# Kernel optimization log

Hardware: AMD Instinct MI355X
Metric: run time of the kernel (lower is better)

Reference implementation:

```python
import jax, jax.numpy as jnp
import numpy as np

N, E, IN, H, OUT, G = 50000, 800000, 128, 256, 10, 512


def setup_inputs() -> dict:
    key = jax.random.key(0)
    ks = jax.random.split(key, 12)
    def lin(k, fan_in, fan_out):
        s = 1.0 / np.sqrt(fan_in)
        kw, kb = jax.random.split(k)
        W = jax.random.uniform(kw, (fan_in, fan_out), jnp.float32, -s, s)
        b = jax.random.uniform(kb, (fan_out,), jnp.float32, -s, s)
        return W, b
    x = jax.random.normal(ks[0], (N, IN), jnp.float32)
    edge_index = jax.random.randint(ks[1], (2, E), 0, N)
    batch = jnp.sort(jax.random.randint(ks[2], (N,), 0, G))
    W1a, b1a = lin(ks[3], IN, H)
    W1b, b1b = lin(ks[4], H, H)
    W2a, b2a = lin(ks[5], H, H)
    W2b, b2b = lin(ks[6], H, H)
    Wlin, blin = lin(ks[7], H, OUT)
    eps1 = jnp.zeros((), jnp.float32)
    eps2 = jnp.zeros((), jnp.float32)
    return dict(x=x, edge_index=edge_index, batch=batch,
                eps1=eps1, W1a=W1a, b1a=b1a, W1b=W1b, b1b=b1b,
                eps2=eps2, W2a=W2a, b2a=b2a, W2b=W2b, b2b=b2b,
                Wlin=Wlin, blin=blin)


def reference(x, edge_index, batch, eps1, W1a, b1a, W1b, b1b,
              eps2, W2a, b2a, W2b, b2b, Wlin, blin):
    src, dst = edge_index[0], edge_index[1]
    # GINConv 1: h = MLP((1+eps)*x + sum_{j in N(i)} x_j)
    agg = jax.ops.segment_sum(x[src], dst, num_segments=N)  # [N, IN]
    h = (1.0 + eps1) * x + agg
    h = jax.nn.relu(h @ W1a + b1a) @ W1b + b1b              # [N, H]
    h = jax.nn.relu(h)  # (dropout p=0.3 is identity in eval mode)
    # GINConv 2
    agg2 = jax.ops.segment_sum(h[src], dst, num_segments=N)  # [N, H]
    h2 = (1.0 + eps2) * h + agg2
    h2 = jax.nn.relu(h2 @ W2a + b2a) @ W2b + b2b             # [N, H]
    # global mean pool per graph
    psum = jax.ops.segment_sum(h2, batch, num_segments=G)    # [G, H]
    cnt = jax.ops.segment_sum(jnp.ones((N, 1), h2.dtype), batch, num_segments=G)
    pooled = psum / jnp.maximum(cnt, 1.0)
    out = pooled @ Wlin + blin                               # [G, OUT]
    return jax.nn.log_softmax(out, axis=-1)
```

## Files before the change

### kernel.cpp

```cpp
#include <hip/hip_runtime.h>
#include <math.h>
#include <stdint.h>

constexpr int N   = 50000;
constexpr int E   = 800000;
constexpr int IN  = 128;
constexpr int H   = 256;
constexpr int OUT = 10;
constexpr int G   = 512;
constexpr int BSTR = 64;

constexpr int NPART  = 391;
constexpr int SEGCAP = 48;
constexpr int EPB    = 4096;
constexpr int AB     = (E + EPB - 1) / EPB;

typedef __bf16 bf16x8 __attribute__((ext_vector_type(8)));
typedef float  f32x4  __attribute__((ext_vector_type(4)));
typedef float  f32x2  __attribute__((ext_vector_type(2)));

__device__ __forceinline__ float blo(unsigned v) { return __uint_as_float(v << 16); }
__device__ __forceinline__ float bhi(unsigned v) { return __uint_as_float(v & 0xffff0000u); }
__device__ __forceinline__ unsigned short f2b(float f) {
  unsigned u = __float_as_uint(f);
  u += 0x7fffu + ((u >> 16) & 1u);
  return (unsigned short)(u >> 16);
}
__device__ __forceinline__ unsigned packb(float lo, float hi) {
  return (unsigned)f2b(lo) | ((unsigned)f2b(hi) << 16);
}
__device__ __forceinline__ unsigned pk_fp8x4(float a, float b, float c, float d) {
  int r = 0;
  r = __builtin_amdgcn_cvt_pk_fp8_f32(a, b, r, false);
  r = __builtin_amdgcn_cvt_pk_fp8_f32(c, d, r, true);
  return (unsigned)r;
}
__device__ __forceinline__ unsigned char fp8_1(float v) {
  return (unsigned char)(__builtin_amdgcn_cvt_pk_fp8_f32(v, v, 0, false) & 0xff);
}

__device__ __forceinline__ void acc16(float* a, uint4 w, float s) {
  unsigned ws[4] = {w.x, w.y, w.z, w.w};
#pragma unroll
  for (int d = 0; d < 4; ++d) {
    f32x2 lo = __builtin_amdgcn_cvt_pk_f32_fp8((int)ws[d], false);
    f32x2 hi = __builtin_amdgcn_cvt_pk_f32_fp8((int)ws[d], true);
    a[4*d+0] = fmaf(s, lo.x, a[4*d+0]);
    a[4*d+1] = fmaf(s, lo.y, a[4*d+1]);
    a[4*d+2] = fmaf(s, hi.x, a[4*d+2]);
    a[4*d+3] = fmaf(s, hi.y, a[4*d+3]);
  }
}


constexpr int XQ_BLOCKS  = (N * IN / 4) / 256;
constexpr int W1A_BLOCKS = (256 * IN) / 256;
constexpr int WH_BLOCKS  = (256 * H) / 256;

__global__ __launch_bounds__(256) void prep_kernel(
    const int* __restrict__ srcp, const int* __restrict__ dstp,
    unsigned* __restrict__ pbuf, int* __restrict__ pcnt,
    const float* __restrict__ x, unsigned* __restrict__ xq,
    const float* __restrict__ W1a, unsigned short* __restrict__ Wt1a,
    const float* __restrict__ W1b, unsigned short* __restrict__ Wt1b,
    const float* __restrict__ W2a, unsigned short* __restrict__ Wt2a,
    const float* __restrict__ W2b, unsigned short* __restrict__ Wt2b) {
  __shared__ int lcur[NPART];
  int b = blockIdx.x;
  int t = threadIdx.x;
  if (b < AB) {
    for (int j = t; j < NPART; j += 256) lcur[j] = 0;
    __syncthreads();
    const int e0 = b * EPB;
#pragma unroll
    for (int r = 0; r < EPB / 1024; ++r) {
      int base = e0 + (r * 256 + t) * 4;
      if (base < E) {
        int4 d4 = *(const int4*)(dstp + base);
        int4 s4 = *(const int4*)(srcp + base);
        int dd[4] = {d4.x, d4.y, d4.z, d4.w};
        int ss[4] = {s4.x, s4.y, s4.z, s4.w};
#pragma unroll
        for (int u = 0; u < 4; ++u) {
          int part = dd[u] >> 7, dl = dd[u] & 127;
          int pos = atomicAdd(&lcur[part], 1);
          if (pos < SEGCAP)
            pbuf[((size_t)part * AB + b) * SEGCAP + pos] =
                ((unsigned)dl << 16) | (unsigned)ss[u];
        }
      }
    }
    __syncthreads();
    for (int j = t; j < NPART; j += 256) pcnt[b * NPART + j] = min(lcur[j], SEGCAP);
    return;
  }
  b -= AB;
  if (b < XQ_BLOCKS) {
    int id = b * 256 + t;
    float4 v = ((const float4*)x)[id];
    xq[id] = pk_fp8x4(v.x, v.y, v.z, v.w);
    return;
  }
  b -= XQ_BLOCKS;
  if (b < W1A_BLOCKS) {
    int id = b * 256 + t;
    int n = id >> 7, k = id & 127;
    Wt1a[id] = f2b(W1a[k * 256 + n]);
    return;
  }
  b -= W1A_BLOCKS;
  const float* Ws;
  unsigned short* Wd;
  if (b < WH_BLOCKS)            { Ws = W1b; Wd = Wt1b; }
  else if (b < 2 * WH_BLOCKS)   { Ws = W2a; Wd = Wt2a; b -= WH_BLOCKS; }
  else                          { Ws = W2b; Wd = Wt2b; b -= 2 * WH_BLOCKS; }
  int id = b * 256 + t;
  int n = id >> 8, k = id & 255;
  Wd[id] = f2b(Ws[k * 256 + n]);
}


__global__ __launch_bounds__(256) void csr_kernel(const unsigned* __restrict__ pbuf,
                                                  const int* __restrict__ pcnt,
                                                  int* __restrict__ deg, int* __restrict__ csre) {
  __shared__ int sa[256], sb[256];
  __shared__ int ldeg[128];
  int p = blockIdx.x;
  int t = threadIdx.x;
  if (t < 128) ldeg[t] = 0;
  sa[t] = (t < AB) ? pcnt[t * NPART + p] : 0;
  __syncthreads();
  int* cur = sa; int* nxt = sb;
#pragma unroll
  for (int off = 1; off < 256; off <<= 1) {
    nxt[t] = cur[t] + ((t >= off) ? cur[t - off] : 0);
    __syncthreads();
    int* tmp = cur; cur = nxt; nxt = tmp;
  }
  int T = cur[255];
  const unsigned* seg = pbuf + (size_t)p * AB * SEGCAP;
  for (int f = t; f < T; f += 256) {
    int lo = 0, hi = AB - 1;
    while (lo < hi) { int m = (lo + hi) >> 1; if (cur[m] > f) hi = m; else lo = m + 1; }
    int bb = lo;
    int excl = bb ? cur[bb - 1] : 0;
    unsigned v = seg[(size_t)bb * SEGCAP + (f - excl)];
    int dl = (int)(v >> 16), s = (int)(v & 0xFFFFu);
    int pos = atomicAdd(&ldeg[dl], 1);
    if (pos < BSTR) csre[(((size_t)p << 7) + dl) * BSTR + pos] = s;
  }
  __syncthreads();
  if (t < 128) {
    int node = (p << 7) + t;
    if (node < N) deg[node] = min(ldeg[t], BSTR);
  }
}


template <int K1, bool RELU2, bool OUT8>
__global__ __launch_bounds__(256, 3) void fused_mlp_kernel(
    const unsigned char* __restrict__ inq,
    const int* __restrict__ deg, const int* __restrict__ csre,
    const float* __restrict__ epsp,
    const unsigned short* __restrict__ Bta,
    const float* __restrict__ ba,
    const unsigned short* __restrict__ Btb,
    const float* __restrict__ bb,
    void* __restrict__ outv, int Nrows) {
  constexpr int LDK = 40;
  constexpr int LDA = K1 + 40;
  constexpr int LDI = H + 40;
  constexpr int W   = K1 / 8;
  constexpr int LPN = W / 16;
  constexpr int BATCH = 8 / LPN;
  __shared__ __align__(16) unsigned short sh[10240 + 32 * LDI];
  unsigned short* Bs = sh;
  unsigned short* Af = sh + 10240;
  unsigned short* Is = sh + 10240;
  const int tid  = threadIdx.x;
  const int r0   = blockIdx.x * 32;
  const int wave = tid >> 6, lane = tid & 63;
  const int quad = lane >> 4, l15 = lane & 15;
  const int wcol = wave * 64;
  const int srow = tid >> 2;
  const int sk8  = (tid & 3) * 8;

  {
    const float sc = 1.0f + epsp[0];
    const int slot = tid & 7;
    const int nd0  = tid >> 3;
    const unsigned char* rb = inq + slot * W;
    const int i = r0 + nd0;
    float a[W];
#pragma unroll
    for (int q = 0; q < W; ++q) a[q] = 0.f;
    if (i < Nrows) {
      int dg = deg[i]; if (dg > BSTR) dg = BSTR;
      const int* bkt = csre + (size_t)i * BSTR;
      int j = 0;
      for (; j + BATCH <= dg; j += BATCH) {
        unsigned idx[BATCH];
#pragma unroll
        for (int u = 0; u < BATCH; ++u) {
          unsigned raw = (unsigned)bkt[j + u];
          idx[u] = raw < (unsigned)N ? raw : 0u;
        }
        uint4 v[8];
#pragma unroll
        for (int u = 0; u < BATCH; ++u) {
          const uint4* src = (const uint4*)(rb + (size_t)idx[u] * K1);
#pragma unroll
          for (int p2 = 0; p2 < LPN; ++p2) v[u * LPN + p2] = src[p2];
        }
#pragma unroll
        for (int u = 0; u < BATCH; ++u)
#pragma unroll
          for (int p2 = 0; p2 < LPN; ++p2) acc16(a + 16 * p2, v[u * LPN + p2], 1.0f);
      }
      for (; j < dg; ++j) {
        unsigned raw = (unsigned)bkt[j];
        if (raw >= (unsigned)N) raw = 0u;
        const uint4* src = (const uint4*)(rb + (size_t)raw * K1);
#pragma unroll
        for (int p2 = 0; p2 < LPN; ++p2) acc16(a + 16 * p2, src[p2], 1.0f);
      }
      const uint4* sr = (const uint4*)(rb + (size_t)i * K1);
#pragma unroll
      for (int p2 = 0; p2 < LPN; ++p2) acc16(a + 16 * p2, sr[p2], sc);
    }
    uint4* dst = (uint4*)(Af + nd0 * LDA + slot * W);
#pragma unroll
    for (int w = 0; w < W / 8; ++w)
      dst[w] = make_uint4(packb(a[8*w+0], a[8*w+1]), packb(a[8*w+2], a[8*w+3]),
                          packb(a[8*w+4], a[8*w+5]), packb(a[8*w+6], a[8*w+7]));
  }

  f32x4 acc1[2][4];
#pragma unroll
  for (int i = 0; i < 2; ++i)
#pragma unroll
    for (int j = 0; j < 4; ++j) acc1[i][j] = (f32x4){0.f, 0.f, 0.f, 0.f};

  for (int k0 = 0; k0 < K1; k0 += 32) {
#pragma unroll
    for (int sgm = 0; sgm < 4; ++sgm) {
      int col = srow + sgm * 64;
      *(uint4*)(Bs + col * LDK + sk8) = *(const uint4*)(Bta + (size_t)col * K1 + k0 + sk8);
    }
    __syncthreads();
    bf16x8 af[2];
#pragma unroll
    for (int mt = 0; mt < 2; ++mt)
      af[mt] = *(const bf16x8*)(Af + (mt * 16 + l15) * LDA + k0 + quad * 8);
    bf16x8 bfr[4];
#pragma unroll
    for (int nt = 0; nt < 4; ++nt)
      bfr[nt] = *(const bf16x8*)(Bs + (wcol + nt * 16 + l15) * LDK + quad * 8);
#pragma unroll
    for (int mt = 0; mt < 2; ++mt)
#pragma unroll
      for (int nt = 0; nt < 4; ++nt)
        acc1[mt][nt] =
            __builtin_amdgcn_mfma_f32_16x16x32_bf16(af[mt], bfr[nt], acc1[mt][nt], 0, 0, 0);
    __syncthreads();
  }

  float bva[4];
#pragma unroll
  for (int nt = 0; nt < 4; ++nt) bva[nt] = ba[wcol + nt * 16 + l15];

#pragma unroll
  for (int mt = 0; mt < 2; ++mt)
#pragma unroll
    for (int nt = 0; nt < 4; ++nt) {
      int col = wcol + nt * 16 + l15;
      int rbase = mt * 16 + quad * 4;
#pragma unroll
      for (int i = 0; i < 4; ++i)
        Is[(rbase + i) * LDI + col] = f2b(fmaxf(acc1[mt][nt][i] + bva[nt], 0.f));
    }
  __syncthreads();

  f32x4 acc2[2][4];
#pragma unroll
  for (int i = 0; i < 2; ++i)
#pragma unroll
    for (int j = 0; j < 4; ++j) acc2[i][j] = (f32x4){0.f, 0.f, 0.f, 0.f};

  for (int kk = 0; kk < H / 32; ++kk) {
    const int k0 = kk * 32;
#pragma unroll
    for (int sgm = 0; sgm < 4; ++sgm) {
      int col = srow + sgm * 64;
      *(uint4*)(Bs + col * LDK + sk8) = *(const uint4*)(Btb + (size_t)col * 256 + k0 + sk8);
    }
    __syncthreads();
    bf16x8 af[2];
#pragma unroll
    for (int mt = 0; mt < 2; ++mt)
      af[mt] = *(const bf16x8*)(Is + (mt * 16 + l15) * LDI + k0 + quad * 8);
    bf16x8 bfr[4];
#pragma unroll
    for (int nt = 0; nt < 4; ++nt)
      bfr[nt] = *(const bf16x8*)(Bs + (wcol + nt * 16 + l15) * LDK + quad * 8);
#pragma unroll
    for (int mt = 0; mt < 2; ++mt)
#pragma unroll
      for (int nt = 0; nt < 4; ++nt)
        acc2[mt][nt] =
            __builtin_amdgcn_mfma_f32_16x16x32_bf16(af[mt], bfr[nt], acc2[mt][nt], 0, 0, 0);
    __syncthreads();
  }

  float bv[4];
#pragma unroll
  for (int nt = 0; nt < 4; ++nt) bv[nt] = bb[wcol + nt * 16 + l15];
#pragma unroll
  for (int mt = 0; mt < 2; ++mt) {
    int gr0 = r0 + mt * 16 + quad * 4;
#pragma unroll
    for (int i = 0; i < 4; ++i) {
      int grow = gr0 + i;
      if (grow >= Nrows) continue;
#pragma unroll
      for (int nt = 0; nt < 4; ++nt) {
        float v = acc2[mt][nt][i] + bv[nt];
        if (RELU2) v = fmaxf(v, 0.f);
        int col = wcol + nt * 16 + l15;
        if (OUT8) ((unsigned char*)outv)[(size_t)grow * 256 + col] = fp8_1(v);
        else      ((unsigned short*)outv)[(size_t)grow * 256 + col] = f2b(v);
      }
    }
  }
}


__global__ __launch_bounds__(128) void pool_final_kernel(const unsigned short* __restrict__ h2,
                                                         const int* __restrict__ batch,
                                                         const float* __restrict__ Wlin,
                                                         const float* __restrict__ blin,
                                                         float* __restrict__ out) {
  __shared__ float sp[H];
  __shared__ float logits[OUT];
  int g = blockIdx.x;
  int t = threadIdx.x;
  int lo = 0, hi = N;
  while (lo < hi) { int m = (lo + hi) >> 1; if (batch[m] < g) lo = m + 1; else hi = m; }
  int s = lo;
  lo = 0; hi = N;
  while (lo < hi) { int m = (lo + hi) >> 1; if (batch[m] < g + 1) lo = m + 1; else hi = m; }
  int e = lo;
  float a0 = 0.f, a1 = 0.f;
  const unsigned* base = (const unsigned*)h2;
  int n = s;
  for (; n + 4 <= e; n += 4) {
    unsigned v0 = base[(size_t)(n + 0) * (H / 2) + t];
    unsigned v1 = base[(size_t)(n + 1) * (H / 2) + t];
    unsigned v2 = base[(size_t)(n + 2) * (H / 2) + t];
    unsigned v3 = base[(size_t)(n + 3) * (H / 2) + t];
    a0 += blo(v0) + blo(v1) + blo(v2) + blo(v3);
    a1 += bhi(v0) + bhi(v1) + bhi(v2) + bhi(v3);
  }
  for (; n < e; ++n) {
    unsigned v = base[(size_t)n * (H / 2) + t];
    a0 += blo(v); a1 += bhi(v);
  }
  float inv = 1.0f / fmaxf((float)(e - s), 1.0f);
  sp[2 * t]     = a0 * inv;
  sp[2 * t + 1] = a1 * inv;
  __syncthreads();
  if (t < OUT) {
    float acc = blin[t];
    for (int k = 0; k < H; ++k) acc = fmaf(sp[k], Wlin[k * OUT + t], acc);
    logits[t] = acc;
  }
  __syncthreads();
  if (t == 0) {
    float m = -INFINITY;
    for (int j = 0; j < OUT; ++j) m = fmaxf(m, logits[j]);
    float ssum = 0.f;
    for (int j = 0; j < OUT; ++j) ssum += expf(logits[j] - m);
    float ls = logf(ssum);
    for (int j = 0; j < OUT; ++j) out[(size_t)g * OUT + j] = logits[j] - m - ls;
  }
}


static inline char* align_up(char* p, size_t a) {
  return (char*)(((uintptr_t)p + a - 1) & ~(a - 1));
}

extern "C" void kernel_launch(void* const* d_in, const int* in_sizes, int n_in,
                              void* d_out, int out_size, void* d_ws, size_t ws_size,
                              hipStream_t stream) {
  const float* x    = (const float*)d_in[0];
  const int*   ei   = (const int*)d_in[1];
  const int*   srcp = ei;
  const int*   dstp = ei + E;
  const int*   batch = (const int*)d_in[2];
  const float* eps1 = (const float*)d_in[3];
  const float* W1a  = (const float*)d_in[4];
  const float* b1a  = (const float*)d_in[5];
  const float* W1b  = (const float*)d_in[6];
  const float* b1b  = (const float*)d_in[7];
  const float* eps2 = (const float*)d_in[8];
  const float* W2a  = (const float*)d_in[9];
  const float* b2a  = (const float*)d_in[10];
  const float* W2b  = (const float*)d_in[11];
  const float* b2b  = (const float*)d_in[12];
  const float* Wlin = (const float*)d_in[13];
  const float* blin = (const float*)d_in[14];
  float* outp = (float*)d_out;

  char* p = (char*)d_ws;
  unsigned* pbuf = (unsigned*)p;     p = align_up(p + (size_t)NPART * AB * SEGCAP * 4, 256);
  int* pcnt = (int*)p;               p = align_up(p + (size_t)AB * NPART * 4, 256);
  int* deg  = (int*)p;               p = align_up(p + (size_t)N * 4, 256);
  int* csre = (int*)p;               p = align_up(p + (size_t)NPART * 128 * BSTR * 4, 256);
  unsigned* xq = (unsigned*)p;       p = align_up(p + (size_t)N * IN, 256);
  unsigned char* h1q = (unsigned char*)p;  p = align_up(p + (size_t)N * H, 256);
  unsigned short* B2 = (unsigned short*)p; p = align_up(p + (size_t)N * H * 2, 256);
  unsigned short* Wt1a = (unsigned short*)p;  p = align_up(p + (size_t)H * IN * 2, 256);
  unsigned short* Wt1b = (unsigned short*)p;  p = align_up(p + (size_t)H * H * 2, 256);
  unsigned short* Wt2a = (unsigned short*)p;  p = align_up(p + (size_t)H * H * 2, 256);
  unsigned short* Wt2b = (unsigned short*)p;  p = align_up(p + (size_t)H * H * 2, 256);

  prep_kernel<<<AB + XQ_BLOCKS + W1A_BLOCKS + 3 * WH_BLOCKS, 256, 0, stream>>>(
      srcp, dstp, pbuf, pcnt, x, xq, W1a, Wt1a, W1b, Wt1b, W2a, Wt2a, W2b, Wt2b);

  csr_kernel<<<NPART, 256, 0, stream>>>(pbuf, pcnt, deg, csre);

  const int nb = (N + 31) / 32;

  fused_mlp_kernel<IN, true, true><<<nb, 256, 0, stream>>>(
      (const unsigned char*)xq, deg, csre, eps1, Wt1a, b1a, Wt1b, b1b, h1q, N);

  fused_mlp_kernel<H, false, false><<<nb, 256, 0, stream>>>(
      h1q, deg, csre, eps2, Wt2a, b2a, Wt2b, b2b, B2, N);

  pool_final_kernel<<<G, 128, 0, stream>>>(B2, batch, Wlin, blin, outp);
}
```

Before: 260.6 us.

## Merge all stages into one cooperative persistent kernel with grid syncs

Replaces the five separate launches (prep, CSR build, two fused GIN MLP layers, pool) with a single cooperative mega-kernel. Blocks loop over virtual block indices for each stage and separate stages with grid.sync(). This removes per-launch overhead and inter-kernel gaps, and falls back to the separate kernels if the cooperative launch fails. In exchange, the persistent grid of 768 blocks caps concurrency per stage, all stages share the largest shared-memory footprint and launch bound, and each grid barrier adds its own cost.

```diff
diff --git a/kernel.cpp b/kernel.cpp
--- a/kernel.cpp
+++ b/kernel.cpp
@@ -1,6 +1,9 @@
 #include <hip/hip_runtime.h>
+#include <hip/hip_cooperative_groups.h>
 #include <math.h>
 #include <stdint.h>
+
+namespace cg = cooperative_groups;
 
 constexpr int N   = 50000;
 constexpr int E   = 800000;
@@ -15,6 +18,14 @@
 constexpr int EPB    = 4096;
 constexpr int AB     = (E + EPB - 1) / EPB;
 
+constexpr int XQ_BLOCKS  = (N * IN / 4) / 256;
+constexpr int W1A_BLOCKS = (256 * IN) / 256;
+constexpr int WH_BLOCKS  = (256 * H) / 256;
+constexpr int PREP_VB    = AB + XQ_BLOCKS + W1A_BLOCKS + 3 * WH_BLOCKS;
+constexpr int NB32       = (N + 31) / 32;
+constexpr int GRID       = 768;
+constexpr int SH_USHORT  = 10240 + 32 * 296;
+
 typedef __bf16 bf16x8 __attribute__((ext_vector_type(8)));
 typedef float  f32x4  __attribute__((ext_vector_type(4)));
 typedef float  f32x2  __attribute__((ext_vector_type(2)));
@@ -52,22 +63,25 @@
   }
 }
 
-
-constexpr int XQ_BLOCKS  = (N * IN / 4) / 256;
-constexpr int W1A_BLOCKS = (256 * IN) / 256;
-constexpr int WH_BLOCKS  = (256 * H) / 256;
-
-__global__ __launch_bounds__(256) void prep_kernel(
-    const int* __restrict__ srcp, const int* __restrict__ dstp,
-    unsigned* __restrict__ pbuf, int* __restrict__ pcnt,
-    const float* __restrict__ x, unsigned* __restrict__ xq,
-    const float* __restrict__ W1a, unsigned short* __restrict__ Wt1a,
-    const float* __restrict__ W1b, unsigned short* __restrict__ Wt1b,
-    const float* __restrict__ W2a, unsigned short* __restrict__ Wt2a,
-    const float* __restrict__ W2b, unsigned short* __restrict__ Wt2b) {
-  __shared__ int lcur[NPART];
-  int b = blockIdx.x;
-  int t = threadIdx.x;
+struct MegaParams {
+  const int* srcp; const int* dstp;
+  unsigned* pbuf; int* pcnt;
+  const float* x; unsigned* xq;
+  const float* W1a; unsigned short* Wt1a;
+  const float* W1b; unsigned short* Wt1b;
+  const float* W2a; unsigned short* Wt2a;
+  const float* W2b; unsigned short* Wt2b;
+  int* deg; int* csre;
+  const float* eps1; const float* eps2;
+  const float* b1a; const float* b1b;
+  const float* b2a; const float* b2b;
+  unsigned char* h1q; unsigned short* B2;
+  const int* batch; const float* Wlin; const float* blin;
+  float* outp;
+};
+
+
+__device__ void prep_vb(int b, int t, const MegaParams& P, int* lcur) {
   if (b < AB) {
     for (int j = t; j < NPART; j += 256) lcur[j] = 0;
     __syncthreads();
@@ -76,8 +90,8 @@
     for (int r = 0; r < EPB / 1024; ++r) {
       int base = e0 + (r * 256 + t) * 4;
       if (base < E) {
-        int4 d4 = *(const int4*)(dstp + base);
-        int4 s4 = *(const int4*)(srcp + base);
+        int4 d4 = *(const int4*)(P.dstp + base);
+        int4 s4 = *(const int4*)(P.srcp + base);
         int dd[4] = {d4.x, d4.y, d4.z, d4.w};
         int ss[4] = {s4.x, s4.y, s4.z, s4.w};
 #pragma unroll
@@ -85,50 +99,48 @@
           int part = dd[u] >> 7, dl = dd[u] & 127;
           int pos = atomicAdd(&lcur[part], 1);
           if (pos < SEGCAP)
-            pbuf[((size_t)part * AB + b) * SEGCAP + pos] =
+            P.pbuf[((size_t)part * AB + b) * SEGCAP + pos] =
                 ((unsigned)dl << 16) | (unsigned)ss[u];
         }
       }
     }
     __syncthreads();
-    for (int j = t; j < NPART; j += 256) pcnt[b * NPART + j] = min(lcur[j], SEGCAP);
+    for (int j = t; j < NPART; j += 256) P.pcnt[b * NPART + j] = min(lcur[j], SEGCAP);
+    __syncthreads();
     return;
   }
   b -= AB;
   if (b < XQ_BLOCKS) {
     int id = b * 256 + t;
-    float4 v = ((const float4*)x)[id];
-    xq[id] = pk_fp8x4(v.x, v.y, v.z, v.w);
+    float4 v = ((const float4*)P.x)[id];
+    P.xq[id] = pk_fp8x4(v.x, v.y, v.z, v.w);
     return;
   }
   b -= XQ_BLOCKS;
   if (b < W1A_BLOCKS) {
     int id = b * 256 + t;
     int n = id >> 7, k = id & 127;
-    Wt1a[id] = f2b(W1a[k * 256 + n]);
+    P.Wt1a[id] = f2b(P.W1a[k * 256 + n]);
     return;
   }
   b -= W1A_BLOCKS;
   const float* Ws;
   unsigned short* Wd;
-  if (b < WH_BLOCKS)            { Ws = W1b; Wd = Wt1b; }
-  else if (b < 2 * WH_BLOCKS)   { Ws = W2a; Wd = Wt2a; b -= WH_BLOCKS; }
-  else                          { Ws = W2b; Wd = Wt2b; b -= 2 * WH_BLOCKS; }
+  if (b < WH_BLOCKS)            { Ws = P.W1b; Wd = P.Wt1b; }
+  else if (b < 2 * WH_BLOCKS)   { Ws = P.W2a; Wd = P.Wt2a; b -= WH_BLOCKS; }
+  else                          { Ws = P.W2b; Wd = P.Wt2b; b -= 2 * WH_BLOCKS; }
   int id = b * 256 + t;
   int n = id >> 8, k = id & 255;
   Wd[id] = f2b(Ws[k * 256 + n]);
 }
 
 
-__global__ __launch_bounds__(256) void csr_kernel(const unsigned* __restrict__ pbuf,
-                                                  const int* __restrict__ pcnt,
-                                                  int* __restrict__ deg, int* __restrict__ csre) {
-  __shared__ int sa[256], sb[256];
-  __shared__ int ldeg[128];
-  int p = blockIdx.x;
-  int t = threadIdx.x;
+__device__ void csr_vb(int p, int t, const MegaParams& P, int* sbuf) {
+  int* sa = sbuf;
+  int* sb = sbuf + 256;
+  int* ldeg = sbuf + 512;
   if (t < 128) ldeg[t] = 0;
-  sa[t] = (t < AB) ? pcnt[t * NPART + p] : 0;
+  sa[t] = (t < AB) ? P.pcnt[t * NPART + p] : 0;
   __syncthreads();
   int* cur = sa; int* nxt = sb;
 #pragma unroll
@@ -138,7 +150,7 @@
     int* tmp = cur; cur = nxt; nxt = tmp;
   }
   int T = cur[255];
-  const unsigned* seg = pbuf + (size_t)p * AB * SEGCAP;
+  const unsigned* seg = P.pbuf + (size_t)p * AB * SEGCAP;
   for (int f = t; f < T; f += 256) {
     int lo = 0, hi = AB - 1;
     while (lo < hi) { int m = (lo + hi) >> 1; if (cur[m] > f) hi = m; else lo = m + 1; }
@@ -147,38 +159,35 @@
     unsigned v = seg[(size_t)bb * SEGCAP + (f - excl)];
     int dl = (int)(v >> 16), s = (int)(v & 0xFFFFu);
     int pos = atomicAdd(&ldeg[dl], 1);
-    if (pos < BSTR) csre[(((size_t)p << 7) + dl) * BSTR + pos] = s;
+    if (pos < BSTR) P.csre[(((size_t)p << 7) + dl) * BSTR + pos] = s;
   }
   __syncthreads();
   if (t < 128) {
     int node = (p << 7) + t;
-    if (node < N) deg[node] = min(ldeg[t], BSTR);
-  }
+    if (node < N) P.deg[node] = min(ldeg[t], BSTR);
+  }
+  __syncthreads();
 }
 
 
 template <int K1, bool RELU2, bool OUT8>
-__global__ __launch_bounds__(256, 3) void fused_mlp_kernel(
+__device__ void fused_tile(int bx, int tid,
     const unsigned char* __restrict__ inq,
     const int* __restrict__ deg, const int* __restrict__ csre,
     const float* __restrict__ epsp,
-    const unsigned short* __restrict__ Bta,
-    const float* __restrict__ ba,
-    const unsigned short* __restrict__ Btb,
-    const float* __restrict__ bb,
-    void* __restrict__ outv, int Nrows) {
+    const unsigned short* __restrict__ Bta, const float* __restrict__ ba,
+    const unsigned short* __restrict__ Btb, const float* __restrict__ bb,
+    void* __restrict__ outv, int Nrows, unsigned short* sh) {
   constexpr int LDK = 40;
   constexpr int LDA = K1 + 40;
   constexpr int LDI = H + 40;
   constexpr int W   = K1 / 8;
   constexpr int LPN = W / 16;
   constexpr int BATCH = 8 / LPN;
-  __shared__ __align__(16) unsigned short sh[10240 + 32 * LDI];
   unsigned short* Bs = sh;
   unsigned short* Af = sh + 10240;
   unsigned short* Is = sh + 10240;
-  const int tid  = threadIdx.x;
-  const int r0   = blockIdx.x * 32;
+  const int r0   = bx * 32;
   const int wave = tid >> 6, lane = tid & 63;
   const int quad = lane >> 4, l15 = lane & 15;
   const int wcol = wave * 64;
@@ -335,43 +344,39 @@
 }
 
 
-__global__ __launch_bounds__(128) void pool_final_kernel(const unsigned short* __restrict__ h2,
-                                                         const int* __restrict__ batch,
-                                                         const float* __restrict__ Wlin,
-                                                         const float* __restrict__ blin,
-                                                         float* __restrict__ out) {
-  __shared__ float sp[H];
-  __shared__ float logits[OUT];
-  int g = blockIdx.x;
-  int t = threadIdx.x;
-  int lo = 0, hi = N;
-  while (lo < hi) { int m = (lo + hi) >> 1; if (batch[m] < g) lo = m + 1; else hi = m; }
-  int s = lo;
-  lo = 0; hi = N;
-  while (lo < hi) { int m = (lo + hi) >> 1; if (batch[m] < g + 1) lo = m + 1; else hi = m; }
-  int e = lo;
-  float a0 = 0.f, a1 = 0.f;
-  const unsigned* base = (const unsigned*)h2;
-  int n = s;
-  for (; n + 4 <= e; n += 4) {
-    unsigned v0 = base[(size_t)(n + 0) * (H / 2) + t];
-    unsigned v1 = base[(size_t)(n + 1) * (H / 2) + t];
-    unsigned v2 = base[(size_t)(n + 2) * (H / 2) + t];
-    unsigned v3 = base[(size_t)(n + 3) * (H / 2) + t];
-    a0 += blo(v0) + blo(v1) + blo(v2) + blo(v3);
-    a1 += bhi(v0) + bhi(v1) + bhi(v2) + bhi(v3);
-  }
-  for (; n < e; ++n) {
-    unsigned v = base[(size_t)n * (H / 2) + t];
-    a0 += blo(v); a1 += bhi(v);
-  }
-  float inv = 1.0f / fmaxf((float)(e - s), 1.0f);
-  sp[2 * t]     = a0 * inv;
-  sp[2 * t + 1] = a1 * inv;
+__device__ void pool_vb(int g, int t, const MegaParams& P, float* sf) {
+  float* sp = sf;
+  float* logits = sf + H;
+  if (t < 128) {
+    int lo = 0, hi = N;
+    while (lo < hi) { int m = (lo + hi) >> 1; if (P.batch[m] < g) lo = m + 1; else hi = m; }
+    int s = lo;
+    lo = 0; hi = N;
+    while (lo < hi) { int m = (lo + hi) >> 1; if (P.batch[m] < g + 1) lo = m + 1; else hi = m; }
+    int e = lo;
+    float a0 = 0.f, a1 = 0.f;
+    const unsigned* base = (const unsigned*)P.B2;
+    int n = s;
+    for (; n + 4 <= e; n += 4) {
+      unsigned v0 = base[(size_t)(n + 0) * (H / 2) + t];
+      unsigned v1 = base[(size_t)(n + 1) * (H / 2) + t];
+      unsigned v2 = base[(size_t)(n + 2) * (H / 2) + t];
+      unsigned v3 = base[(size_t)(n + 3) * (H / 2) + t];
+      a0 += blo(v0) + blo(v1) + blo(v2) + blo(v3);
+      a1 += bhi(v0) + bhi(v1) + bhi(v2) + bhi(v3);
+    }
+    for (; n < e; ++n) {
+      unsigned v = base[(size_t)n * (H / 2) + t];
+      a0 += blo(v); a1 += bhi(v);
+    }
+    float inv = 1.0f / fmaxf((float)(e - s), 1.0f);
+    sp[2 * t]     = a0 * inv;
+    sp[2 * t + 1] = a1 * inv;
+  }
   __syncthreads();
   if (t < OUT) {
-    float acc = blin[t];
-    for (int k = 0; k < H; ++k) acc = fmaf(sp[k], Wlin[k * OUT + t], acc);
+    float acc = P.blin[t];
+    for (int k = 0; k < H; ++k) acc = fmaf(sp[k], P.Wlin[k * OUT + t], acc);
     logits[t] = acc;
   }
   __syncthreads();
@@ -381,8 +386,57 @@
     float ssum = 0.f;
     for (int j = 0; j < OUT; ++j) ssum += expf(logits[j] - m);
     float ls = logf(ssum);
-    for (int j = 0; j < OUT; ++j) out[(size_t)g * OUT + j] = logits[j] - m - ls;
-  }
+    for (int j = 0; j < OUT; ++j) P.outp[(size_t)g * OUT + j] = logits[j] - m - ls;
+  }
+  __syncthreads();
+}
+
+
+__global__ __launch_bounds__(256, 3) void mega_kernel(MegaParams P) {
+  __shared__ __align__(16) unsigned short sh[SH_USHORT];
+  const int t = threadIdx.x;
+  cg::grid_group grid = cg::this_grid();
+
+  for (int vb = blockIdx.x; vb < PREP_VB; vb += gridDim.x)
+    prep_vb(vb, t, P, (int*)sh);
+  grid.sync();
+  for (int vb = blockIdx.x; vb < NPART; vb += gridDim.x)
+    csr_vb(vb, t, P, (int*)sh);
+  grid.sync();
+  for (int vb = blockIdx.x; vb < NB32; vb += gridDim.x)
+    fused_tile<IN, true, true>(vb, t, (const unsigned char*)P.xq, P.deg, P.csre, P.eps1,
+                               P.Wt1a, P.b1a, P.Wt1b, P.b1b, P.h1q, N, sh);
+  grid.sync();
+  for (int vb = blockIdx.x; vb < NB32; vb += gridDim.x)
+    fused_tile<H, false, false>(vb, t, P.h1q, P.deg, P.csre, P.eps2,
+                                P.Wt2a, P.b2a, P.Wt2b, P.b2b, P.B2, N, sh);
+  grid.sync();
+  for (int vb = blockIdx.x; vb < G; vb += gridDim.x)
+    pool_vb(vb, t, P, (float*)sh);
+}
+
+
+__global__ __launch_bounds__(256) void prep_k(MegaParams P) {
+  __shared__ int lcur[NPART];
+  prep_vb(blockIdx.x, threadIdx.x, P, lcur);
+}
+__global__ __launch_bounds__(256) void csr_k(MegaParams P) {
+  __shared__ int sbuf[640];
+  csr_vb(blockIdx.x, threadIdx.x, P, sbuf);
+}
+template <int K1>
+__global__ __launch_bounds__(256, 3) void fused_k(MegaParams P) {
+  __shared__ __align__(16) unsigned short sh[SH_USHORT];
+  if constexpr (K1 == IN)
+    fused_tile<IN, true, true>(blockIdx.x, threadIdx.x, (const unsigned char*)P.xq, P.deg,
+                               P.csre, P.eps1, P.Wt1a, P.b1a, P.Wt1b, P.b1b, P.h1q, N, sh);
+  else
+    fused_tile<H, false, false>(blockIdx.x, threadIdx.x, P.h1q, P.deg,
+                                P.csre, P.eps2, P.Wt2a, P.b2a, P.Wt2b, P.b2b, P.B2, N, sh);
+}
+__global__ __launch_bounds__(256) void pool_k(MegaParams P) {
+  __shared__ float sf[H + OUT];
+  pool_vb(blockIdx.x, threadIdx.x, P, sf);
 }
 
 
@@ -393,24 +447,7 @@
 extern "C" void kernel_launch(void* const* d_in, const int* in_sizes, int n_in,
                               void* d_out, int out_size, void* d_ws, size_t ws_size,
                               hipStream_t stream) {
-  const float* x    = (const float*)d_in[0];
-  const int*   ei   = (const int*)d_in[1];
-  const int*   srcp = ei;
-  const int*   dstp = ei + E;
-  const int*   batch = (const int*)d_in[2];
-  const float* eps1 = (const float*)d_in[3];
-  const float* W1a  = (const float*)d_in[4];
-  const float* b1a  = (const float*)d_in[5];
-  const float* W1b  = (const float*)d_in[6];
-  const float* b1b  = (const float*)d_in[7];
-  const float* eps2 = (const float*)d_in[8];
-  const float* W2a  = (const float*)d_in[9];
-  const float* b2a  = (const float*)d_in[10];
-  const float* W2b  = (const float*)d_in[11];
-  const float* b2b  = (const float*)d_in[12];
-  const float* Wlin = (const float*)d_in[13];
-  const float* blin = (const float*)d_in[14];
-  float* outp = (float*)d_out;
+  const int* ei = (const int*)d_in[1];
 
   char* p = (char*)d_ws;
   unsigned* pbuf = (unsigned*)p;     p = align_up(p + (size_t)NPART * AB * SEGCAP * 4, 256);
@@ -425,18 +462,32 @@
   unsigned short* Wt2a = (unsigned short*)p;  p = align_up(p + (size_t)H * H * 2, 256);
   unsigned short* Wt2b = (unsigned short*)p;  p = align_up(p + (size_t)H * H * 2, 256);
 
-  prep_kernel<<<AB + XQ_BLOCKS + W1A_BLOCKS + 3 * WH_BLOCKS, 256, 0, stream>>>(
-      srcp, dstp, pbuf, pcnt, x, xq, W1a, Wt1a, W1b, Wt1b, W2a, Wt2a, W2b, Wt2b);
-
-  csr_kernel<<<NPART, 256, 0, stream>>>(pbuf, pcnt, deg, csre);
-
-  const int nb = (N + 31) / 32;
-
-  fused_mlp_kernel<IN, true, true><<<nb, 256, 0, stream>>>(
-      (const unsigned char*)xq, deg, csre, eps1, Wt1a, b1a, Wt1b, b1b, h1q, N);
-
-  fused_mlp_kernel<H, false, false><<<nb, 256, 0, stream>>>(
-      h1q, deg, csre, eps2, Wt2a, b2a, Wt2b, b2b, B2, N);
-
-  pool_final_kernel<<<G, 128, 0, stream>>>(B2, batch, Wlin, blin, outp);
-}
+  MegaParams mp;
+  mp.srcp = ei;                 mp.dstp = ei + E;
+  mp.pbuf = pbuf;               mp.pcnt = pcnt;
+  mp.x    = (const float*)d_in[0];   mp.xq = xq;
+  mp.W1a  = (const float*)d_in[4];   mp.Wt1a = Wt1a;
+  mp.W1b  = (const float*)d_in[6];   mp.Wt1b = Wt1b;
+  mp.W2a  = (const float*)d_in[9];   mp.Wt2a = Wt2a;
+  mp.W2b  = (const float*)d_in[11];  mp.Wt2b = Wt2b;
+  mp.deg  = deg;                mp.csre = csre;
+  mp.eps1 = (const float*)d_in[3];   mp.eps2 = (const float*)d_in[8];
+  mp.b1a  = (const float*)d_in[5];   mp.b1b  = (const float*)d_in[7];
+  mp.b2a  = (const float*)d_in[10];  mp.b2b  = (const float*)d_in[12];
+  mp.h1q  = h1q;                mp.B2 = B2;
+  mp.batch = (const int*)d_in[2];
+  mp.Wlin = (const float*)d_in[13];  mp.blin = (const float*)d_in[14];
+  mp.outp = (float*)d_out;
+
+  void* kp[] = { (void*)&mp };
+  hipError_t ce = hipLaunchCooperativeKernel((const void*)mega_kernel,
+                                             dim3(GRID), dim3(256), kp, 0, stream);
+  if (ce != hipSuccess) {
+    (void)hipGetLastError();
+    prep_k<<<PREP_VB, 256, 0, stream>>>(mp);
+    csr_k<<<NPART, 256, 0, stream>>>(mp);
+    fused_k<IN><<<NB32, 256, 0, stream>>>(mp);
+    fused_k<H><<<NB32, 256, 0, stream>>>(mp);
+    pool_k<<<G, 256, 0, stream>>>(mp);
+  }
+}
```

New measurement: 802.7 us. +208.0%, slower.
